# Performance work log

Measured on AMD Instinct MI355X. Metric: run time of the kernel, lower is better.

The kernel has to match this reference:

```python
import math
import jax, jax.numpy as jnp
import numpy as np

B, N, D, H = 4, 2048, 512, 8
HD = D // H


def setup_inputs() -> dict:
    key = jax.random.key(0)
    ks = jax.random.split(key, 7)
    w_scale = 1.0 / math.sqrt(D)  # keep logits in a sane range (like default init)
    return {
        "q": jax.random.normal(ks[0], (B, N, D), dtype=jnp.float32),
        "mask": jax.random.randint(ks[1], (B, N), 0, 2) == 1,  # True = masked key
        "attn_bias": jax.random.normal(ks[2], (B, N, N), dtype=jnp.float32),
        "Wq": jax.random.normal(ks[3], (D, D), dtype=jnp.float32) * w_scale,
        "Wk": jax.random.normal(ks[4], (D, D), dtype=jnp.float32) * w_scale,
        "Wv": jax.random.normal(ks[5], (D, D), dtype=jnp.float32) * w_scale,
        "Wo": jax.random.normal(ks[6], (D, D), dtype=jnp.float32) * w_scale,
    }


def _heads(v):
    # [B, N, D] -> [H, B, N, HD]  (mirrors reshape + movedim(-2, 0))
    b, n, d = v.shape
    return v.reshape(b, n, H, HD).transpose(2, 0, 1, 3)


def reference(q, mask, attn_bias, Wq, Wk, Wv, Wo):
    # Linear projections (torch Linear: x @ W.T)
    qh = _heads(q @ Wq.T)
    kh = _heads(q @ Wk.T)   # self-attention: h defaults to q
    vh = _heads(q @ Wv.T)
    # scores: [H, B, Nq, Nk]
    scores = jnp.einsum("hbqd,hbkd->hbqk", qh, kh) / math.sqrt(HD)
    scores = scores + attn_bias[None]                     # broadcast over heads
    scores = jnp.where(mask[None, :, None, :], -jnp.inf, scores)
    attn = jax.nn.softmax(scores, axis=-1)
    out = jnp.einsum("hbqk,hbkd->hbqd", attn, vh)         # [H, B, Nq, HD]
    out = out.transpose(1, 2, 0, 3).reshape(q.shape[0], q.shape[1], D)
    return out @ Wo.T
```

## Files before the change

kernel.cpp:

```cpp
#include <hip/hip_runtime.h>
#include <stdint.h>


typedef __attribute__((ext_vector_type(8))) short short8;
typedef __attribute__((ext_vector_type(4))) short short4v;
typedef __attribute__((ext_vector_type(4))) float f32x4;

#define DEV static __device__ __forceinline__

constexpr int Bc = 4, Nc = 2048, Dc = 512, Hc = 8, HDc = 64;
constexpr int Mc = Bc * Nc;
constexpr int QKVNc = 3 * Dc;
constexpr float L2E = 1.44269504f;

DEV short bf16cast(float f) {
  return (short)__builtin_bit_cast(unsigned short, (__bf16)f);
}
DEV unsigned cvt_pk_bf16(float a, float b) {
  unsigned short lb = __builtin_bit_cast(unsigned short, (__bf16)a);
  unsigned short hb = __builtin_bit_cast(unsigned short, (__bf16)b);
  return (unsigned)lb | ((unsigned)hb << 16);
}
DEV unsigned pack_shorts(short a, short b) {
  return (unsigned)(unsigned short)a | ((unsigned)(unsigned short)b << 16);
}
DEV short8 cvt8(float4 a, float4 b) {
  union { short8 s; uint4 u; } r;
  r.u.x = cvt_pk_bf16(a.x, a.y); r.u.y = cvt_pk_bf16(a.z, a.w);
  r.u.z = cvt_pk_bf16(b.x, b.y); r.u.w = cvt_pk_bf16(b.z, b.w);
  return r.s;
}
DEV float fast_exp2(float x) {
#if __has_builtin(__builtin_amdgcn_exp2f)
  return __builtin_amdgcn_exp2f(x);
#else
  return exp2f(x);
#endif
}
DEV void permswap32(unsigned& a, unsigned& b) {
  asm volatile("v_permlane32_swap_b32 %0, %1" : "+v"(a), "+v"(b));
}
DEV void gl_lds16(const short* g, short* l) {
  __builtin_amdgcn_global_load_lds(
      (const __attribute__((address_space(1))) void*)g,
      (__attribute__((address_space(3))) void*)l, 16, 0, 0);
}
DEV void barrier_lgkm_only() {
  asm volatile("s_waitcnt lgkmcnt(0)" ::: "memory");
  __builtin_amdgcn_s_barrier();
  __builtin_amdgcn_sched_barrier(0);
}

__global__ void cvtw_kernel(const float* __restrict__ Wq, const float* __restrict__ Wk,
                            const float* __restrict__ Wv, const float* __restrict__ Wo,
                            short* __restrict__ Wqkv, short* __restrict__ Wob) {
  int which = blockIdx.x >> 8;
  int j = (blockIdx.x & 255) * 256 + threadIdx.x;
  const float* src = which == 0 ? Wq : which == 1 ? Wk : which == 2 ? Wv : Wo;
  short* dst = (which == 3) ? Wob : Wqkv + which * (Dc * Dc);
  float4 v = ((const float4*)src)[j];
  short4v o = { bf16cast(v.x), bf16cast(v.y), bf16cast(v.z), bf16cast(v.w) };
  ((short4v*)dst)[j] = o;
}

__global__ __launch_bounds__(256, 2) void gemm_qkv(const float* __restrict__ q,
                                                   const short* __restrict__ Wqkv,
                                                   short* __restrict__ QKV,
                                                   float cscale) {
  constexpr int K = 512;
  __shared__ __align__(16) short At[128 * 72];
  __shared__ __align__(16) short Bt[2][192 * 64];
  const int tid = threadIdx.x, lane = tid & 63, wv = tid >> 6;
  const int quad = lane >> 4, l16 = lane & 15;
  const int mbase = blockIdx.y * 128, nbase = blockIdx.x * 192;
  const int wr = (wv >> 1) * 64, wc = (wv & 1) * 96;
  f32x4 acc[4][6] = {};
  float4 apf[4][2];
#pragma unroll
  for (int i = 0; i < 4; i++) {
    int flat = i * 256 + tid, row = flat >> 3, ch8 = (flat & 7) * 8;
    apf[i][0] = *(const float4*)&q[(size_t)(mbase + row) * K + ch8];
    apf[i][1] = *(const float4*)&q[(size_t)(mbase + row) * K + ch8 + 4];
  }
#pragma unroll
  for (int i = 0; i < 6; i++) {
    int ibase = (wv * 6 + i) * 64;
    int row = (ibase + lane) >> 3, ch = lane & 7;
    gl_lds16(&Wqkv[(size_t)(nbase + row) * K + ((ch ^ (row & 7)) << 3)],
             &Bt[0][ibase << 3]);
  }
  for (int k0 = 0; k0 < K; k0 += 64) {
    const int cur = (k0 >> 6) & 1;
    __syncthreads();
#pragma unroll
    for (int i = 0; i < 4; i++) {
      int flat = i * 256 + tid, row = flat >> 3, ch8 = (flat & 7) * 8;
      *(short8*)&At[row * 72 + ch8] = cvt8(apf[i][0], apf[i][1]);
    }
    if (k0 + 64 < K) {
#pragma unroll
      for (int i = 0; i < 6; i++) {
        int ibase = (wv * 6 + i) * 64;
        int row = (ibase + lane) >> 3, ch = lane & 7;
        gl_lds16(&Wqkv[(size_t)(nbase + row) * K + k0 + 64 + ((ch ^ (row & 7)) << 3)],
                 &Bt[cur ^ 1][ibase << 3]);
      }
#pragma unroll
      for (int i = 0; i < 4; i++) {
        int flat = i * 256 + tid, row = flat >> 3, ch8 = (flat & 7) * 8;
        apf[i][0] = *(const float4*)&q[(size_t)(mbase + row) * K + k0 + 64 + ch8];
        apf[i][1] = *(const float4*)&q[(size_t)(mbase + row) * K + k0 + 64 + ch8 + 4];
      }
    }
    barrier_lgkm_only();
#pragma unroll
    for (int s = 0; s < 2; s++) {
      short8 af[4], bf[6];
#pragma unroll
      for (int t = 0; t < 4; t++)
        af[t] = *(short8*)&At[(wr + t * 16 + l16) * 72 + quad * 8 + s * 32];
#pragma unroll
      for (int t = 0; t < 6; t++) {
        int r = wc + t * 16 + l16;
        bf[t] = *(short8*)&Bt[cur][r * 64 + (((quad + 4 * s) ^ (r & 7)) << 3)];
      }
#pragma unroll
      for (int mt = 0; mt < 4; mt++)
#pragma unroll
        for (int nt = 0; nt < 6; nt++)
          acc[mt][nt] = __builtin_amdgcn_mfma_f32_16x16x32_bf16(af[mt], bf[nt], acc[mt][nt], 0, 0, 0);
    }
  }
#pragma unroll
  for (int nt = 0; nt < 6; nt++) {
    const float sc = (nbase + wc + nt * 16 < 512) ? cscale : 1.0f;
#pragma unroll
    for (int mt = 0; mt < 4; mt++)
#pragma unroll
      for (int r = 0; r < 4; r++) {
        int row = mbase + wr + mt * 16 + quad * 4 + r;
        int col = nbase + wc + nt * 16 + l16;
        QKV[(size_t)row * QKVNc + col] = bf16cast(acc[mt][nt][r] * sc);
      }
  }
}

__global__ __launch_bounds__(256, 2) void gemm_out(const short* __restrict__ aout,
                                                   const short* __restrict__ Wob,
                                                   float* __restrict__ out) {
  constexpr int K = 512;
  __shared__ __align__(16) short At[2][128 * 64];
  __shared__ __align__(16) short Bt[2][64 * 64];
  const int tid = threadIdx.x, lane = tid & 63, wv = tid >> 6;
  const int quad = lane >> 4, l16 = lane & 15;
  const int mbase = blockIdx.y * 128, nbase = blockIdx.x * 64;
  const int wr = wv * 32;
  f32x4 acc[2][4] = {};
#pragma unroll
  for (int i = 0; i < 4; i++) {
    int ibase = (wv * 4 + i) * 64;
    int row = (ibase + lane) >> 3, ch = lane & 7;
    gl_lds16(&aout[(size_t)(mbase + row) * K + ((ch ^ (row & 7)) << 3)],
             &At[0][ibase << 3]);
  }
#pragma unroll
  for (int i = 0; i < 2; i++) {
    int ibase = (wv * 2 + i) * 64;
    int row = (ibase + lane) >> 3, ch = lane & 7;
    gl_lds16(&Wob[(size_t)(nbase + row) * K + ((ch ^ (row & 7)) << 3)],
             &Bt[0][ibase << 3]);
  }
  for (int k0 = 0; k0 < K; k0 += 64) {
    const int cur = (k0 >> 6) & 1;
    __syncthreads();
    if (k0 + 64 < K) {
#pragma unroll
      for (int i = 0; i < 4; i++) {
        int ibase = (wv * 4 + i) * 64;
        int row = (ibase + lane) >> 3, ch = lane & 7;
        gl_lds16(&aout[(size_t)(mbase + row) * K + k0 + 64 + ((ch ^ (row & 7)) << 3)],
                 &At[cur ^ 1][ibase << 3]);
      }
#pragma unroll
      for (int i = 0; i < 2; i++) {
        int ibase = (wv * 2 + i) * 64;
        int row = (ibase + lane) >> 3, ch = lane & 7;
        gl_lds16(&Wob[(size_t)(nbase + row) * K + k0 + 64 + ((ch ^ (row & 7)) << 3)],
                 &Bt[cur ^ 1][ibase << 3]);
      }
    }
#pragma unroll
    for (int s = 0; s < 2; s++) {
      short8 af[2], bf[4];
#pragma unroll
      for (int t = 0; t < 2; t++) {
        int r = wr + t * 16 + l16;
        af[t] = *(short8*)&At[cur][r * 64 + (((quad + 4 * s) ^ (r & 7)) << 3)];
      }
#pragma unroll
      for (int t = 0; t < 4; t++) {
        int r = t * 16 + l16;
        bf[t] = *(short8*)&Bt[cur][r * 64 + (((quad + 4 * s) ^ (r & 7)) << 3)];
      }
#pragma unroll
      for (int mt = 0; mt < 2; mt++)
#pragma unroll
        for (int nt = 0; nt < 4; nt++)
          acc[mt][nt] = __builtin_amdgcn_mfma_f32_16x16x32_bf16(af[mt], bf[nt], acc[mt][nt], 0, 0, 0);
    }
  }
#pragma unroll
  for (int mt = 0; mt < 2; mt++)
#pragma unroll
    for (int nt = 0; nt < 4; nt++)
#pragma unroll
      for (int r = 0; r < 4; r++) {
        int row = mbase + wr + mt * 16 + quad * 4 + r;
        int col = nbase + nt * 16 + l16;
        out[(size_t)row * Dc + col] = acc[mt][nt][r];
      }
}

__global__ __launch_bounds__(256, 2) void attn_kernel(const short* __restrict__ QKV,
                                                      const float* __restrict__ bias,
                                                      const void* __restrict__ mask,
                                                      short* __restrict__ Aout) {
  __shared__ __align__(16) short Kt[4][64 * 64];
  __shared__ __align__(16) short Vt[4][64 * 64];
  __shared__ __align__(16) float mlds[Nc];
  __shared__ int mflag;
  const int tid = threadIdx.x, lane = tid & 63, wv = tid >> 6;
  const int quad = lane >> 4, l16 = lane & 15;
  const int qt = blockIdx.x & 15, h = (blockIdx.x >> 4) & 7, b = (int)(blockIdx.x >> 7);
  const int qrow0 = qt * 128;
  const int q0 = qrow0 + wv * 32 + l16;
  const float* biasq0 = bias + ((size_t)b * Nc + q0) * Nc;
  const float* biasq1 = biasq0 + (size_t)16 * Nc;
  const short* Kbase = QKV + Dc + h * HDc;
  const short* Vbase = QKV + 2 * Dc + h * HDc;

#pragma unroll
  for (int j = 0; j < 2; j++)
#pragma unroll
    for (int g = 0; g < 2; g++) {
      int seg = wv * 2 + g, c = seg * 64 + lane;
      int row = c >> 3, ch = c & 7;
      gl_lds16(&Kbase[(size_t)(b * Nc + j * 64 + row) * QKVNc + ((ch ^ (row & 7)) << 3)],
               &Kt[j][seg * 512]);
    }

  short8 qf[2][2];
  {
    const short* qp0 = QKV + (size_t)(b * Nc + q0) * QKVNc + h * HDc + quad * 8;
    qf[0][0] = *(const short8*)qp0;
    qf[0][1] = *(const short8*)(qp0 + 32);
    const short* qp1 = qp0 + (size_t)16 * QKVNc;
    qf[1][0] = *(const short8*)qp1;
    qf[1][1] = *(const short8*)(qp1 + 32);
  }

  const int vp = tid & 31, vq = tid >> 5;
  const int vperm = (vp & 25) | ((vp & 4) >> 1) | ((vp & 2) << 1);
  const int vwbase = (((vperm >> 2)) << 3) + 2 * (vperm & 3);

  short8 v0pre[2], v1pre[2];
  float4 bpre[2][2][4];
#pragma unroll
  for (int j = 0; j < 2; j++) {
    v0pre[j] = *(const short8*)&Vbase[(size_t)(b * Nc + j * 64 + 2 * vp) * QKVNc + vq * 8];
    v1pre[j] = *(const short8*)&Vbase[(size_t)(b * Nc + j * 64 + 2 * vp + 1) * QKVNc + vq * 8];
#pragma unroll
    for (int t = 0; t < 4; t++) {
      bpre[j][0][t] = *(const float4*)&biasq0[j * 64 + t * 16 + quad * 4];
      bpre[j][1][t] = *(const float4*)&biasq1[j * 64 + t * 16 + quad * 4];
    }
  }

  if (tid == 0) mflag = 0;
  __syncthreads();
  {
    const uchar4* mw = (const uchar4*)((const char*)mask + (size_t)b * 2048);
    int acc = 0;
#pragma unroll
    for (int i = tid; i < 512; i += 256) {
      uchar4 v = mw[i];
      acc |= (int)v.y | (int)v.z | (int)v.w;
    }
    if (acc) atomicOr(&mflag, 1);
  }
  __syncthreads();
  {
    int isbyte = mflag;
    const unsigned char* mb = (const unsigned char*)mask + (size_t)b * 2048;
    const int* mi = (const int*)mask + (size_t)b * 2048;
    for (int i = tid; i < Nc; i += 256) {
      int v = isbyte ? (int)mb[i] : mi[i];
      mlds[i] = v ? -1e30f : 0.0f;
    }
  }

  const short ONEB = (short)0x3F80;
  const short8 ones = { ONEB, ONEB, ONEB, ONEB, ONEB, ONEB, ONEB, ONEB };

  f32x4 oacc[2][4] = {};
  f32x4 sumacc[2] = {};

  for (int pd = 0; pd < 16; pd++) {
    const int pb = (pd & 1) * 2;
    const int nb = 2 - pb;

#pragma unroll
    for (int j = 0; j < 2; j++)
#pragma unroll
      for (int jj = 0; jj < 8; jj++) {
        int hd = vq * 8 + jj;
        *(unsigned*)&Vt[pb + j][hd * 64 + (vwbase ^ ((hd & 7) << 3))] =
            pack_shorts(v0pre[j][jj], v1pre[j][jj]);
      }
    __syncthreads();

#pragma unroll
    for (int j = 0; j < 2; j++) {
      const int kn = ((2 * pd + 2 + j) & 31) * 64;
#pragma unroll
      for (int g = 0; g < 2; g++) {
        int seg = wv * 2 + g, c = seg * 64 + lane;
        int row = c >> 3, ch = c & 7;
        gl_lds16(&Kbase[(size_t)(b * Nc + kn + row) * QKVNc + ((ch ^ (row & 7)) << 3)],
                 &Kt[nb + j][seg * 512]);
      }
      v0pre[j] = *(const short8*)&Vbase[(size_t)(b * Nc + kn + 2 * vp) * QKVNc + vq * 8];
      v1pre[j] = *(const short8*)&Vbase[(size_t)(b * Nc + kn + 2 * vp + 1) * QKVNc + vq * 8];
    }

#pragma unroll
    for (int j = 0; j < 2; j++) {
      const int kb = (2 * pd + j) * 64;
      const int knb = ((2 * pd + j + 2) & 31) * 64;

      f32x4 sacc[2][4];
#pragma unroll
      for (int t = 0; t < 4; t++) {
        float4 mv = *(const float4*)&mlds[kb + t * 16 + quad * 4];
        sacc[0][t][0] = mv.x; sacc[0][t][1] = mv.y; sacc[0][t][2] = mv.z; sacc[0][t][3] = mv.w;
        sacc[1][t] = sacc[0][t];
      }

      __builtin_amdgcn_s_setprio(1);
#pragma unroll
      for (int s = 0; s < 2; s++)
#pragma unroll
        for (int t = 0; t < 4; t++) {
          short8 kf = *(short8*)&Kt[pb + j][(t * 16 + l16) * 64 + (((quad + 4 * s) ^ (l16 & 7)) << 3)];
          sacc[0][t] = __builtin_amdgcn_mfma_f32_16x16x32_bf16(kf, qf[0][s], sacc[0][t], 0, 0, 0);
          sacc[1][t] = __builtin_amdgcn_mfma_f32_16x16x32_bf16(kf, qf[1][s], sacc[1][t], 0, 0, 0);
        }
      __builtin_amdgcn_s_setprio(0);

      short8 pf[2][2];
#pragma unroll
      for (int n = 0; n < 2; n++) {
        unsigned pw[4][2];
#pragma unroll
        for (int t = 0; t < 4; t++) {
          float p0 = fast_exp2(__builtin_fmaf(bpre[j][n][t].x, L2E, sacc[n][t][0]));
          float p1 = fast_exp2(__builtin_fmaf(bpre[j][n][t].y, L2E, sacc[n][t][1]));
          float p2 = fast_exp2(__builtin_fmaf(bpre[j][n][t].z, L2E, sacc[n][t][2]));
          float p3 = fast_exp2(__builtin_fmaf(bpre[j][n][t].w, L2E, sacc[n][t][3]));
          pw[t][0] = cvt_pk_bf16(p0, p1);
          pw[t][1] = cvt_pk_bf16(p2, p3);
        }
        permswap32(pw[0][0], pw[1][0]); permswap32(pw[0][1], pw[1][1]);
        permswap32(pw[2][0], pw[3][0]); permswap32(pw[2][1], pw[3][1]);
        union { unsigned u[4]; short8 s; }
            a0{{pw[0][0], pw[0][1], pw[1][0], pw[1][1]}},
            a1{{pw[2][0], pw[2][1], pw[3][0], pw[3][1]}};
        pf[n][0] = a0.s; pf[n][1] = a1.s;
      }

#pragma unroll
      for (int t = 0; t < 4; t++) {
        bpre[j][0][t] = *(const float4*)&biasq0[knb + t * 16 + quad * 4];
        bpre[j][1][t] = *(const float4*)&biasq1[knb + t * 16 + quad * 4];
      }

      __builtin_amdgcn_s_setprio(1);
#pragma unroll
      for (int s = 0; s < 2; s++) {
        sumacc[0] = __builtin_amdgcn_mfma_f32_16x16x32_bf16(pf[0][s], ones, sumacc[0], 0, 0, 0);
        sumacc[1] = __builtin_amdgcn_mfma_f32_16x16x32_bf16(pf[1][s], ones, sumacc[1], 0, 0, 0);
#pragma unroll
        for (int t = 0; t < 4; t++) {
          short8 vf = *(short8*)&Vt[pb + j][(t * 16 + l16) * 64 + (((quad + 4 * s) ^ (l16 & 7)) << 3)];
          oacc[0][t] = __builtin_amdgcn_mfma_f32_16x16x32_bf16(pf[0][s], vf, oacc[0][t], 0, 0, 0);
          oacc[1][t] = __builtin_amdgcn_mfma_f32_16x16x32_bf16(pf[1][s], vf, oacc[1][t], 0, 0, 0);
        }
      }
      __builtin_amdgcn_s_setprio(0);
    }
  }

#pragma unroll
  for (int m = 0; m < 2; m++)
#pragma unroll
    for (int r = 0; r < 4; r++) {
      float inv = 1.0f / sumacc[m][r];
      int row = b * Nc + qrow0 + wv * 32 + m * 16 + quad * 4 + r;
#pragma unroll
      for (int t = 0; t < 4; t++)
        Aout[(size_t)row * Dc + h * HDc + t * 16 + l16] = bf16cast(oacc[m][t][r] * inv);
    }
}

extern "C" void kernel_launch(void* const* d_in, const int* in_sizes, int n_in,
                              void* d_out, int out_size, void* d_ws, size_t ws_size,
                              hipStream_t stream) {
  const float* q    = (const float*)d_in[0];
  const void*  mask = d_in[1];
  const float* bias = (const float*)d_in[2];
  const float* Wq   = (const float*)d_in[3];
  const float* Wk   = (const float*)d_in[4];
  const float* Wv   = (const float*)d_in[5];
  const float* Wo   = (const float*)d_in[6];
  float* out = (float*)d_out;

  char* ws = (char*)d_ws;
  short* Wqkv = (short*)ws;  ws += (size_t)QKVNc * Dc * 2;
  short* Wob  = (short*)ws;  ws += (size_t)Dc * Dc * 2;
  short* QKV  = (short*)ws;  ws += (size_t)Mc * QKVNc * 2;
  short* aout = (short*)ws;  ws += (size_t)Mc * Dc * 2;

  cvtw_kernel<<<dim3(1024), dim3(256), 0, stream>>>(Wq, Wk, Wv, Wo, Wqkv, Wob);

  gemm_qkv<<<dim3(QKVNc / 192, Mc / 128), dim3(256), 0, stream>>>(
      q, Wqkv, QKV, 0.125f * L2E);
  attn_kernel<<<dim3(Bc * Hc * 16), dim3(256), 0, stream>>>(QKV, bias, mask, aout);
  gemm_out<<<dim3(Dc / 64, Mc / 128), dim3(256), 0, stream>>>(aout, Wob, out);
}
```

Baseline: 244.4 us.

## Share bias tile across head pairs in attention; pre-convert q to bf16

The attention kernel now runs 512 threads per block and covers two heads per block. The shared bias+mask tile is loaded once into LDS in premultiplied form and reused by both heads, which halves the global bias traffic. Separately, the input q is converted to bf16 in the weight-conversion kernel, so the QKV GEMM can load A through direct global-to-LDS copies with double buffering instead of register conversion. The cost is more LDS per block, fewer blocks, an extra bf16 copy of q in the workspace, and the removal of the lgkm-only barrier.

```diff
diff --git a/kernel.cpp b/kernel.cpp
--- a/kernel.cpp
+++ b/kernel.cpp
@@ -23,12 +23,6 @@
 }
 DEV unsigned pack_shorts(short a, short b) {
   return (unsigned)(unsigned short)a | ((unsigned)(unsigned short)b << 16);
-}
-DEV short8 cvt8(float4 a, float4 b) {
-  union { short8 s; uint4 u; } r;
-  r.u.x = cvt_pk_bf16(a.x, a.y); r.u.y = cvt_pk_bf16(a.z, a.w);
-  r.u.z = cvt_pk_bf16(b.x, b.y); r.u.w = cvt_pk_bf16(b.z, b.w);
-  return r.s;
 }
 DEV float fast_exp2(float x) {
 #if __has_builtin(__builtin_amdgcn_exp2f)
@@ -45,42 +39,46 @@
       (const __attribute__((address_space(1))) void*)g,
       (__attribute__((address_space(3))) void*)l, 16, 0, 0);
 }
-DEV void barrier_lgkm_only() {
-  asm volatile("s_waitcnt lgkmcnt(0)" ::: "memory");
-  __builtin_amdgcn_s_barrier();
-  __builtin_amdgcn_sched_barrier(0);
-}
 
 __global__ void cvtw_kernel(const float* __restrict__ Wq, const float* __restrict__ Wk,
                             const float* __restrict__ Wv, const float* __restrict__ Wo,
-                            short* __restrict__ Wqkv, short* __restrict__ Wob) {
-  int which = blockIdx.x >> 8;
-  int j = (blockIdx.x & 255) * 256 + threadIdx.x;
-  const float* src = which == 0 ? Wq : which == 1 ? Wk : which == 2 ? Wv : Wo;
-  short* dst = (which == 3) ? Wob : Wqkv + which * (Dc * Dc);
+                            const float* __restrict__ q,
+                            short* __restrict__ Wqkv, short* __restrict__ Wob,
+                            short* __restrict__ qb) {
+  int bid = blockIdx.x;
+  const float* src; short* dst; int j;
+  if (bid < 1024) {
+    int which = bid >> 8;
+    j = (bid & 255) * 256 + threadIdx.x;
+    src = which == 0 ? Wq : which == 1 ? Wk : which == 2 ? Wv : Wo;
+    dst = (which == 3) ? Wob : Wqkv + which * (Dc * Dc);
+  } else {
+    j = (bid - 1024) * 256 + threadIdx.x;
+    src = q; dst = qb;
+  }
   float4 v = ((const float4*)src)[j];
   short4v o = { bf16cast(v.x), bf16cast(v.y), bf16cast(v.z), bf16cast(v.w) };
   ((short4v*)dst)[j] = o;
 }
 
-__global__ __launch_bounds__(256, 2) void gemm_qkv(const float* __restrict__ q,
+__global__ __launch_bounds__(256, 2) void gemm_qkv(const short* __restrict__ qb,
                                                    const short* __restrict__ Wqkv,
                                                    short* __restrict__ QKV,
                                                    float cscale) {
   constexpr int K = 512;
-  __shared__ __align__(16) short At[128 * 72];
+  __shared__ __align__(16) short At[2][128 * 64];
   __shared__ __align__(16) short Bt[2][192 * 64];
   const int tid = threadIdx.x, lane = tid & 63, wv = tid >> 6;
   const int quad = lane >> 4, l16 = lane & 15;
   const int mbase = blockIdx.y * 128, nbase = blockIdx.x * 192;
   const int wr = (wv >> 1) * 64, wc = (wv & 1) * 96;
   f32x4 acc[4][6] = {};
-  float4 apf[4][2];
 #pragma unroll
   for (int i = 0; i < 4; i++) {
-    int flat = i * 256 + tid, row = flat >> 3, ch8 = (flat & 7) * 8;
-    apf[i][0] = *(const float4*)&q[(size_t)(mbase + row) * K + ch8];
-    apf[i][1] = *(const float4*)&q[(size_t)(mbase + row) * K + ch8 + 4];
+    int ibase = (wv * 4 + i) * 64;
+    int row = (ibase + lane) >> 3, ch = lane & 7;
+    gl_lds16(&qb[(size_t)(mbase + row) * K + ((ch ^ (row & 7)) << 3)],
+             &At[0][ibase << 3]);
   }
 #pragma unroll
   for (int i = 0; i < 6; i++) {
@@ -92,12 +90,14 @@
   for (int k0 = 0; k0 < K; k0 += 64) {
     const int cur = (k0 >> 6) & 1;
     __syncthreads();
-#pragma unroll
-    for (int i = 0; i < 4; i++) {
-      int flat = i * 256 + tid, row = flat >> 3, ch8 = (flat & 7) * 8;
-      *(short8*)&At[row * 72 + ch8] = cvt8(apf[i][0], apf[i][1]);
-    }
     if (k0 + 64 < K) {
+#pragma unroll
+      for (int i = 0; i < 4; i++) {
+        int ibase = (wv * 4 + i) * 64;
+        int row = (ibase + lane) >> 3, ch = lane & 7;
+        gl_lds16(&qb[(size_t)(mbase + row) * K + k0 + 64 + ((ch ^ (row & 7)) << 3)],
+                 &At[cur ^ 1][ibase << 3]);
+      }
 #pragma unroll
       for (int i = 0; i < 6; i++) {
         int ibase = (wv * 6 + i) * 64;
@@ -105,20 +105,15 @@
         gl_lds16(&Wqkv[(size_t)(nbase + row) * K + k0 + 64 + ((ch ^ (row & 7)) << 3)],
                  &Bt[cur ^ 1][ibase << 3]);
       }
-#pragma unroll
-      for (int i = 0; i < 4; i++) {
-        int flat = i * 256 + tid, row = flat >> 3, ch8 = (flat & 7) * 8;
-        apf[i][0] = *(const float4*)&q[(size_t)(mbase + row) * K + k0 + 64 + ch8];
-        apf[i][1] = *(const float4*)&q[(size_t)(mbase + row) * K + k0 + 64 + ch8 + 4];
-      }
-    }
-    barrier_lgkm_only();
+    }
 #pragma unroll
     for (int s = 0; s < 2; s++) {
       short8 af[4], bf[6];
 #pragma unroll
-      for (int t = 0; t < 4; t++)
-        af[t] = *(short8*)&At[(wr + t * 16 + l16) * 72 + quad * 8 + s * 32];
+      for (int t = 0; t < 4; t++) {
+        int r = wr + t * 16 + l16;
+        af[t] = *(short8*)&At[cur][r * 64 + (((quad + 4 * s) ^ (r & 7)) << 3)];
+      }
 #pragma unroll
       for (int t = 0; t < 6; t++) {
         int r = wc + t * 16 + l16;
@@ -221,33 +216,33 @@
       }
 }
 
-__global__ __launch_bounds__(256, 2) void attn_kernel(const short* __restrict__ QKV,
+__global__ __launch_bounds__(512, 2) void attn_kernel(const short* __restrict__ QKV,
                                                       const float* __restrict__ bias,
                                                       const void* __restrict__ mask,
                                                       short* __restrict__ Aout) {
-  __shared__ __align__(16) short Kt[4][64 * 64];
-  __shared__ __align__(16) short Vt[4][64 * 64];
+  __shared__ __align__(16) short Kt[2][2][64 * 64];
+  __shared__ __align__(16) short Vt[2][2][64 * 64];
+  __shared__ __align__(16) float blds[2][128 * 68];
   __shared__ __align__(16) float mlds[Nc];
   __shared__ int mflag;
   const int tid = threadIdx.x, lane = tid & 63, wv = tid >> 6;
   const int quad = lane >> 4, l16 = lane & 15;
-  const int qt = blockIdx.x & 15, h = (blockIdx.x >> 4) & 7, b = (int)(blockIdx.x >> 7);
+  const int hp = blockIdx.x & 3, qt = (blockIdx.x >> 2) & 15, b = (int)(blockIdx.x >> 6);
+  const int hw = wv >> 2;
+  const int h = hp * 2 + hw;
+  const int wq = wv & 3;
   const int qrow0 = qt * 128;
-  const int q0 = qrow0 + wv * 32 + l16;
-  const float* biasq0 = bias + ((size_t)b * Nc + q0) * Nc;
-  const float* biasq1 = biasq0 + (size_t)16 * Nc;
+  const int q0 = qrow0 + wq * 32 + l16;
   const short* Kbase = QKV + Dc + h * HDc;
   const short* Vbase = QKV + 2 * Dc + h * HDc;
 
 #pragma unroll
-  for (int j = 0; j < 2; j++)
-#pragma unroll
-    for (int g = 0; g < 2; g++) {
-      int seg = wv * 2 + g, c = seg * 64 + lane;
-      int row = c >> 3, ch = c & 7;
-      gl_lds16(&Kbase[(size_t)(b * Nc + j * 64 + row) * QKVNc + ((ch ^ (row & 7)) << 3)],
-               &Kt[j][seg * 512]);
-    }
+  for (int g = 0; g < 2; g++) {
+    int seg = (wv & 3) * 2 + g, c = seg * 64 + lane;
+    int row = c >> 3, ch = c & 7;
+    gl_lds16(&Kbase[(size_t)(b * Nc + row) * QKVNc + ((ch ^ (row & 7)) << 3)],
+             &Kt[hw][0][seg * 512]);
+  }
 
   short8 qf[2][2];
   {
@@ -259,30 +254,27 @@
     qf[1][1] = *(const short8*)(qp1 + 32);
   }
 
-  const int vp = tid & 31, vq = tid >> 5;
+  const int lt = tid & 255;
+  const int vp = lt & 31, vq = lt >> 5;
   const int vperm = (vp & 25) | ((vp & 4) >> 1) | ((vp & 2) << 1);
   const int vwbase = (((vperm >> 2)) << 3) + 2 * (vperm & 3);
 
-  short8 v0pre[2], v1pre[2];
-  float4 bpre[2][2][4];
-#pragma unroll
-  for (int j = 0; j < 2; j++) {
-    v0pre[j] = *(const short8*)&Vbase[(size_t)(b * Nc + j * 64 + 2 * vp) * QKVNc + vq * 8];
-    v1pre[j] = *(const short8*)&Vbase[(size_t)(b * Nc + j * 64 + 2 * vp + 1) * QKVNc + vq * 8];
-#pragma unroll
-    for (int t = 0; t < 4; t++) {
-      bpre[j][0][t] = *(const float4*)&biasq0[j * 64 + t * 16 + quad * 4];
-      bpre[j][1][t] = *(const float4*)&biasq1[j * 64 + t * 16 + quad * 4];
-    }
-  }
+  short8 v0pre, v1pre;
+  v0pre = *(const short8*)&Vbase[(size_t)(b * Nc + 2 * vp) * QKVNc + vq * 8];
+  v1pre = *(const short8*)&Vbase[(size_t)(b * Nc + 2 * vp + 1) * QKVNc + vq * 8];
+
+  const int bq = tid >> 2, bc4 = (tid & 3) * 16;
+  const float* biasP = bias + ((size_t)b * Nc + qrow0 + bq) * Nc;
+  float4 bpre[4];
+#pragma unroll
+  for (int j = 0; j < 4; j++) bpre[j] = *(const float4*)&biasP[bc4 + 4 * j];
 
   if (tid == 0) mflag = 0;
   __syncthreads();
   {
     const uchar4* mw = (const uchar4*)((const char*)mask + (size_t)b * 2048);
     int acc = 0;
-#pragma unroll
-    for (int i = tid; i < 512; i += 256) {
+    for (int i = tid; i < 512; i += 512) {
       uchar4 v = mw[i];
       acc |= (int)v.y | (int)v.z | (int)v.w;
     }
@@ -293,7 +285,7 @@
     int isbyte = mflag;
     const unsigned char* mb = (const unsigned char*)mask + (size_t)b * 2048;
     const int* mi = (const int*)mask + (size_t)b * 2048;
-    for (int i = tid; i < Nc; i += 256) {
+    for (int i = tid; i < Nc; i += 512) {
       int v = isbyte ? (int)mb[i] : mi[i];
       mlds[i] = v ? -1e30f : 0.0f;
     }
@@ -305,99 +297,90 @@
   f32x4 oacc[2][4] = {};
   f32x4 sumacc[2] = {};
 
-  for (int pd = 0; pd < 16; pd++) {
-    const int pb = (pd & 1) * 2;
-    const int nb = 2 - pb;
-
-#pragma unroll
-    for (int j = 0; j < 2; j++)
-#pragma unroll
-      for (int jj = 0; jj < 8; jj++) {
-        int hd = vq * 8 + jj;
-        *(unsigned*)&Vt[pb + j][hd * 64 + (vwbase ^ ((hd & 7) << 3))] =
-            pack_shorts(v0pre[j][jj], v1pre[j][jj]);
-      }
+  for (int kt = 0; kt < 32; kt++) {
+    const int cur = kt & 1;
+    const int kb = kt * 64;
+    const int kbn = ((kt + 1) & 31) * 64;
+
+#pragma unroll
+    for (int jj = 0; jj < 8; jj++) {
+      int hd = vq * 8 + jj;
+      *(unsigned*)&Vt[hw][cur][hd * 64 + (vwbase ^ ((hd & 7) << 3))] =
+          pack_shorts(v0pre[jj], v1pre[jj]);
+    }
+#pragma unroll
+    for (int j = 0; j < 4; j++) {
+      float4 m = *(const float4*)&mlds[kb + bc4 + 4 * j];
+      float4 o = { __builtin_fmaf(bpre[j].x, L2E, m.x), __builtin_fmaf(bpre[j].y, L2E, m.y),
+                   __builtin_fmaf(bpre[j].z, L2E, m.z), __builtin_fmaf(bpre[j].w, L2E, m.w) };
+      *(float4*)&blds[cur][bq * 68 + bc4 + 4 * j] = o;
+    }
     __syncthreads();
 
 #pragma unroll
-    for (int j = 0; j < 2; j++) {
-      const int kn = ((2 * pd + 2 + j) & 31) * 64;
-#pragma unroll
-      for (int g = 0; g < 2; g++) {
-        int seg = wv * 2 + g, c = seg * 64 + lane;
-        int row = c >> 3, ch = c & 7;
-        gl_lds16(&Kbase[(size_t)(b * Nc + kn + row) * QKVNc + ((ch ^ (row & 7)) << 3)],
-                 &Kt[nb + j][seg * 512]);
-      }
-      v0pre[j] = *(const short8*)&Vbase[(size_t)(b * Nc + kn + 2 * vp) * QKVNc + vq * 8];
-      v1pre[j] = *(const short8*)&Vbase[(size_t)(b * Nc + kn + 2 * vp + 1) * QKVNc + vq * 8];
-    }
-
-#pragma unroll
-    for (int j = 0; j < 2; j++) {
-      const int kb = (2 * pd + j) * 64;
-      const int knb = ((2 * pd + j + 2) & 31) * 64;
-
-      f32x4 sacc[2][4];
+    for (int g = 0; g < 2; g++) {
+      int seg = (wv & 3) * 2 + g, c = seg * 64 + lane;
+      int row = c >> 3, ch = c & 7;
+      gl_lds16(&Kbase[(size_t)(b * Nc + kbn + row) * QKVNc + ((ch ^ (row & 7)) << 3)],
+               &Kt[hw][cur ^ 1][seg * 512]);
+    }
+    v0pre = *(const short8*)&Vbase[(size_t)(b * Nc + kbn + 2 * vp) * QKVNc + vq * 8];
+    v1pre = *(const short8*)&Vbase[(size_t)(b * Nc + kbn + 2 * vp + 1) * QKVNc + vq * 8];
+#pragma unroll
+    for (int j = 0; j < 4; j++) bpre[j] = *(const float4*)&biasP[kbn + bc4 + 4 * j];
+
+    f32x4 sacc[2][4];
+#pragma unroll
+    for (int n = 0; n < 2; n++)
+#pragma unroll
+      for (int t = 0; t < 4; t++)
+        sacc[n][t] = *(f32x4*)&blds[cur][(wq * 32 + n * 16 + l16) * 68 + t * 16 + quad * 4];
+
+    __builtin_amdgcn_s_setprio(1);
+#pragma unroll
+    for (int s = 0; s < 2; s++)
 #pragma unroll
       for (int t = 0; t < 4; t++) {
-        float4 mv = *(const float4*)&mlds[kb + t * 16 + quad * 4];
-        sacc[0][t][0] = mv.x; sacc[0][t][1] = mv.y; sacc[0][t][2] = mv.z; sacc[0][t][3] = mv.w;
-        sacc[1][t] = sacc[0][t];
-      }
-
-      __builtin_amdgcn_s_setprio(1);
-#pragma unroll
-      for (int s = 0; s < 2; s++)
-#pragma unroll
-        for (int t = 0; t < 4; t++) {
-          short8 kf = *(short8*)&Kt[pb + j][(t * 16 + l16) * 64 + (((quad + 4 * s) ^ (l16 & 7)) << 3)];
-          sacc[0][t] = __builtin_amdgcn_mfma_f32_16x16x32_bf16(kf, qf[0][s], sacc[0][t], 0, 0, 0);
-          sacc[1][t] = __builtin_amdgcn_mfma_f32_16x16x32_bf16(kf, qf[1][s], sacc[1][t], 0, 0, 0);
-        }
-      __builtin_amdgcn_s_setprio(0);
-
-      short8 pf[2][2];
-#pragma unroll
-      for (int n = 0; n < 2; n++) {
-        unsigned pw[4][2];
-#pragma unroll
-        for (int t = 0; t < 4; t++) {
-          float p0 = fast_exp2(__builtin_fmaf(bpre[j][n][t].x, L2E, sacc[n][t][0]));
-          float p1 = fast_exp2(__builtin_fmaf(bpre[j][n][t].y, L2E, sacc[n][t][1]));
-          float p2 = fast_exp2(__builtin_fmaf(bpre[j][n][t].z, L2E, sacc[n][t][2]));
-          float p3 = fast_exp2(__builtin_fmaf(bpre[j][n][t].w, L2E, sacc[n][t][3]));
-          pw[t][0] = cvt_pk_bf16(p0, p1);
-          pw[t][1] = cvt_pk_bf16(p2, p3);
-        }
-        permswap32(pw[0][0], pw[1][0]); permswap32(pw[0][1], pw[1][1]);
-        permswap32(pw[2][0], pw[3][0]); permswap32(pw[2][1], pw[3][1]);
-        union { unsigned u[4]; short8 s; }
-            a0{{pw[0][0], pw[0][1], pw[1][0], pw[1][1]}},
-            a1{{pw[2][0], pw[2][1], pw[3][0], pw[3][1]}};
-        pf[n][0] = a0.s; pf[n][1] = a1.s;
-      }
-
+        short8 kf = *(short8*)&Kt[hw][cur][(t * 16 + l16) * 64 + (((quad + 4 * s) ^ (l16 & 7)) << 3)];
+        sacc[0][t] = __builtin_amdgcn_mfma_f32_16x16x32_bf16(kf, qf[0][s], sacc[0][t], 0, 0, 0);
+        sacc[1][t] = __builtin_amdgcn_mfma_f32_16x16x32_bf16(kf, qf[1][s], sacc[1][t], 0, 0, 0);
+      }
+    __builtin_amdgcn_s_setprio(0);
+
+    short8 pf[2][2];
+#pragma unroll
+    for (int n = 0; n < 2; n++) {
+      unsigned pw[4][2];
 #pragma unroll
       for (int t = 0; t < 4; t++) {
-        bpre[j][0][t] = *(const float4*)&biasq0[knb + t * 16 + quad * 4];
-        bpre[j][1][t] = *(const float4*)&biasq1[knb + t * 16 + quad * 4];
-      }
-
-      __builtin_amdgcn_s_setprio(1);
-#pragma unroll
-      for (int s = 0; s < 2; s++) {
-        sumacc[0] = __builtin_amdgcn_mfma_f32_16x16x32_bf16(pf[0][s], ones, sumacc[0], 0, 0, 0);
-        sumacc[1] = __builtin_amdgcn_mfma_f32_16x16x32_bf16(pf[1][s], ones, sumacc[1], 0, 0, 0);
-#pragma unroll
-        for (int t = 0; t < 4; t++) {
-          short8 vf = *(short8*)&Vt[pb + j][(t * 16 + l16) * 64 + (((quad + 4 * s) ^ (l16 & 7)) << 3)];
-          oacc[0][t] = __builtin_amdgcn_mfma_f32_16x16x32_bf16(pf[0][s], vf, oacc[0][t], 0, 0, 0);
-          oacc[1][t] = __builtin_amdgcn_mfma_f32_16x16x32_bf16(pf[1][s], vf, oacc[1][t], 0, 0, 0);
-        }
-      }
-      __builtin_amdgcn_s_setprio(0);
-    }
+        float p0 = fast_exp2(sacc[n][t][0]);
+        float p1 = fast_exp2(sacc[n][t][1]);
+        float p2 = fast_exp2(sacc[n][t][2]);
+        float p3 = fast_exp2(sacc[n][t][3]);
+        pw[t][0] = cvt_pk_bf16(p0, p1);
+        pw[t][1] = cvt_pk_bf16(p2, p3);
+      }
+      permswap32(pw[0][0], pw[1][0]); permswap32(pw[0][1], pw[1][1]);
+      permswap32(pw[2][0], pw[3][0]); permswap32(pw[2][1], pw[3][1]);
+      union { unsigned u[4]; short8 s; }
+          a0{{pw[0][0], pw[0][1], pw[1][0], pw[1][1]}},
+          a1{{pw[2][0], pw[2][1], pw[3][0], pw[3][1]}};
+      pf[n][0] = a0.s; pf[n][1] = a1.s;
+    }
+
+    __builtin_amdgcn_s_setprio(1);
+#pragma unroll
+    for (int s = 0; s < 2; s++) {
+      sumacc[0] = __builtin_amdgcn_mfma_f32_16x16x32_bf16(pf[0][s], ones, sumacc[0], 0, 0, 0);
+      sumacc[1] = __builtin_amdgcn_mfma_f32_16x16x32_bf16(pf[1][s], ones, sumacc[1], 0, 0, 0);
+#pragma unroll
+      for (int t = 0; t < 4; t++) {
+        short8 vf = *(short8*)&Vt[hw][cur][(t * 16 + l16) * 64 + (((quad + 4 * s) ^ (l16 & 7)) << 3)];
+        oacc[0][t] = __builtin_amdgcn_mfma_f32_16x16x32_bf16(pf[0][s], vf, oacc[0][t], 0, 0, 0);
+        oacc[1][t] = __builtin_amdgcn_mfma_f32_16x16x32_bf16(pf[1][s], vf, oacc[1][t], 0, 0, 0);
+      }
+    }
+    __builtin_amdgcn_s_setprio(0);
   }
 
 #pragma unroll
@@ -405,7 +388,7 @@
 #pragma unroll
     for (int r = 0; r < 4; r++) {
       float inv = 1.0f / sumacc[m][r];
-      int row = b * Nc + qrow0 + wv * 32 + m * 16 + quad * 4 + r;
+      int row = b * Nc + qrow0 + wq * 32 + m * 16 + quad * 4 + r;
 #pragma unroll
       for (int t = 0; t < 4; t++)
         Aout[(size_t)row * Dc + h * HDc + t * 16 + l16] = bf16cast(oacc[m][t][r] * inv);
@@ -427,13 +410,14 @@
   char* ws = (char*)d_ws;
   short* Wqkv = (short*)ws;  ws += (size_t)QKVNc * Dc * 2;
   short* Wob  = (short*)ws;  ws += (size_t)Dc * Dc * 2;
+  short* qb   = (short*)ws;  ws += (size_t)Mc * Dc * 2;
   short* QKV  = (short*)ws;  ws += (size_t)Mc * QKVNc * 2;
   short* aout = (short*)ws;  ws += (size_t)Mc * Dc * 2;
 
-  cvtw_kernel<<<dim3(1024), dim3(256), 0, stream>>>(Wq, Wk, Wv, Wo, Wqkv, Wob);
+  cvtw_kernel<<<dim3(5120), dim3(256), 0, stream>>>(Wq, Wk, Wv, Wo, q, Wqkv, Wob, qb);
 
   gemm_qkv<<<dim3(QKVNc / 192, Mc / 128), dim3(256), 0, stream>>>(
-      q, Wqkv, QKV, 0.125f * L2E);
-  attn_kernel<<<dim3(Bc * Hc * 16), dim3(256), 0, stream>>>(QKV, bias, mask, aout);
+      qb, Wqkv, QKV, 0.125f * L2E);
+  attn_kernel<<<dim3(Bc * 16 * 4), dim3(512), 0, stream>>>(QKV, bias, mask, aout);
   gemm_out<<<dim3(Dc / 64, Mc / 128), dim3(256), 0, stream>>>(aout, Wob, out);
 }
```

After: 251.6 us. 3.0% more time.
